# Performance work log

Hardware: AMD Instinct MI355X
Metric: run time of the kernel (lower is better)

## Reference

```python
import jax, jax.numpy as jnp
import numpy as np

N_NODES = 100000
N_EDGES = 1600000
NFEAT, NHID, NCLASS = 128, 64, 40


def setup_inputs() -> dict:
    key = jax.random.key(0)
    k = jax.random.split(key, 6)
    x = jax.random.normal(k[0], (N_NODES, NFEAT), dtype=jnp.float32)
    edge_index = jax.random.randint(k[1], (2, N_EDGES), 0, N_NODES, dtype=jnp.int64)
    edge_weight = jax.random.uniform(k[2], (N_EDGES,), dtype=jnp.float32)
    # Glorot-style init as in PyG GCNConv.reset_parameters
    W1 = jax.random.normal(k[3], (NFEAT, NHID), dtype=jnp.float32) * (1.0 / np.sqrt(NFEAT))
    b1 = jnp.zeros((NHID,), dtype=jnp.float32)
    W2 = jax.random.normal(k[4], (NHID, NCLASS), dtype=jnp.float32) * (1.0 / np.sqrt(NHID))
    b2 = jnp.zeros((NCLASS,), dtype=jnp.float32)
    return {"x": x, "edge_index": edge_index, "edge_weight": edge_weight,
            "W1": W1, "b1": b1, "W2": W2, "b2": b2}


def _gcn_conv(x, edge_index, edge_weight, W, b):
    """PyG GCNConv: add self-loops, symmetric gcn_norm, linear, scatter-add, bias."""
    n = x.shape[0]
    loop = jnp.arange(n)
    row = jnp.concatenate([edge_index[0], loop])  # source nodes
    col = jnp.concatenate([edge_index[1], loop])  # target nodes
    w = jnp.concatenate([edge_weight, jnp.ones((n,), edge_weight.dtype)])
    deg = jax.ops.segment_sum(w, col, num_segments=n)          # [N]
    dinv = jnp.where(deg > 0, jax.lax.rsqrt(deg), 0.0)
    norm = dinv[row] * w * dinv[col]                           # [E+N]
    h = x @ W                                                  # [N, out]
    msg = norm[:, None] * h[row]                               # gather: [E+N, out]
    out = jax.ops.segment_sum(msg, col, num_segments=n)        # scatter-add: [N, out]
    return out + b


def reference(x, edge_index, edge_weight, W1, b1, W2, b2):
    h = jax.nn.relu(_gcn_conv(x, edge_index, edge_weight, W1, b1))
    # F.dropout with training=False is identity (eval mode)
    return _gcn_conv(h, edge_index, edge_weight, W2, b2)
```

## Files before the change

### kernel.cpp

```cpp
#include <hip/hip_runtime.h>
#include <hip/hip_bf16.h>

#define N_NODES 100000
#define N_EDGES 1600000
#define NFEAT 128
#define NHID 64
#define NCLASS 40
#define CAP 64

#define BIN_SHIFT 9
#define BIN_NODES 512
#define NBIN ((N_NODES + BIN_NODES - 1) / BIN_NODES)
#define SCAP 10240
#define CHUNK 4096
#define EPT 16

using frag_ab = __attribute__((ext_vector_type(8))) short;
using frag_cd = __attribute__((ext_vector_type(4))) float;


__device__ __forceinline__ unsigned pack2(float a, float b) {
    unsigned ua = __float_as_uint(a), ub = __float_as_uint(b);
    unsigned ra = (ua + 0x7FFFu + ((ua >> 16) & 1u)) >> 16;
    unsigned rb = (ub + 0x7FFFu + ((ub >> 16) & 1u)) >> 16;
    return ra | (rb << 16);
}
__device__ __forceinline__ unsigned short bf16rtn(float f) {
    unsigned u = __float_as_uint(f);
    return (unsigned short)((u + 0x7FFFu + ((u >> 16) & 1u)) >> 16);
}
__device__ __forceinline__ float lo16(unsigned w) { return __uint_as_float(w << 16); }
__device__ __forceinline__ float hi16(unsigned w) { return __uint_as_float(w & 0xFFFF0000u); }


__global__ __launch_bounds__(256) void bin_kernel(const int* __restrict__ ei,
                                                  const float* __restrict__ ew,
                                                  int* __restrict__ bincnt,
                                                  uint2* __restrict__ staging) {
    __shared__ int lcnt[NBIN];
    __shared__ int gbase[NBIN];
    int t = threadIdx.x;
    for (int i = t; i < NBIN; i += 256) lcnt[i] = 0;
    __syncthreads();

    int base = blockIdx.x * CHUNK;
    int c[EPT]; unsigned en[EPT];
#pragma unroll
    for (int u = 0; u < EPT; ++u) {
        int e = base + u * 256 + t;
        if (e < N_EDGES) {
            c[u] = ei[N_EDGES + e];
            unsigned wq = (unsigned)fminf(ew[e] * 32768.0f, 32767.0f);
            en[u] = ((unsigned)ei[e] << 15) | wq;
        } else {
            c[u] = -1;
        }
    }
#pragma unroll
    for (int u = 0; u < EPT; ++u)
        if (c[u] >= 0) atomicAdd(&lcnt[c[u] >> BIN_SHIFT], 1);
    __syncthreads();
    if (t < NBIN) {
        int n = lcnt[t];
        gbase[t] = (n > 0) ? atomicAdd(&bincnt[t], n) : 0;
    }
    __syncthreads();
    if (t < NBIN) lcnt[t] = 0;
    __syncthreads();
#pragma unroll
    for (int u = 0; u < EPT; ++u) {
        if (c[u] >= 0) {
            int b = c[u] >> BIN_SHIFT;
            int p = gbase[b] + atomicAdd(&lcnt[b], 1);
            if (p < SCAP)
                staging[(size_t)b * SCAP + p] = make_uint2(en[u], (unsigned)c[u]);
        }
    }
}


__global__ __launch_bounds__(512) void place_kernel(const int* __restrict__ bincnt,
                                                    const uint2* __restrict__ staging,
                                                    unsigned* __restrict__ bucket,
                                                    int* __restrict__ cnt,
                                                    float* __restrict__ dinv) {
    __shared__ int lpos[BIN_NODES];
    __shared__ float lws[BIN_NODES];
    int b = blockIdx.x;
    int t = threadIdx.x;
    for (int i = t; i < BIN_NODES; i += 512) { lpos[i] = 0; lws[i] = 0.0f; }
    __syncthreads();

    int nodebase = b << BIN_SHIFT;
    int n = bincnt[b];
    if (n > SCAP) n = SCAP;
    const uint2* st = staging + (size_t)b * SCAP;
    for (int i = t; i < n; i += 512) {
        uint2 en = st[i];
        int local = (int)en.y - nodebase;
        int p = atomicAdd(&lpos[local], 1);
        if (p < CAP) bucket[((size_t)en.y << 6) + p] = en.x;
        atomicAdd(&lws[local], (float)(en.x & 32767u) * (1.0f / 32768.0f));
    }
    __syncthreads();
    for (int i = t; i < BIN_NODES; i += 512) {
        int node = nodebase + i;
        if (node < N_NODES) {
            cnt[node] = min(lpos[i], CAP);
            dinv[node] = rsqrtf(1.0f + lws[i]);
        }
    }
}


__global__ __launch_bounds__(256) void gemm1_kernel(const float* __restrict__ x,
                                                    const float* __restrict__ W1,
                                                    unsigned short* __restrict__ h1b) {
    __shared__ unsigned short sm[16384];
    int t = threadIdx.x;
    int row0 = blockIdx.x * 64;

#pragma unroll
    for (int p = 0; p < 4; ++p) {
        int id = p * 256 + t;
        int r = id >> 4;
        int c = id & 15;
        int gr = row0 + r; if (gr > N_NODES - 1) gr = N_NODES - 1;
        const float* src = x + (size_t)gr * NFEAT + c * 8;
        float4 f0 = *(const float4*)src;
        float4 f1 = *(const float4*)(src + 4);
        uint4 pk = make_uint4(pack2(f0.x, f0.y), pack2(f0.z, f0.w),
                              pack2(f1.x, f1.y), pack2(f1.z, f1.w));
        int cs = c ^ (r & 15);
        *(uint4*)(&sm[r * 128 + cs * 8]) = pk;
    }
#pragma unroll
    for (int p = 0; p < 4; ++p) {
        int id = p * 256 + t;
        int n = id >> 4;
        int c = id & 15;
        const float* wsrc = W1 + (size_t)(c * 8) * NHID + n;
        uint4 pk = make_uint4(pack2(wsrc[0 * NHID], wsrc[1 * NHID]),
                              pack2(wsrc[2 * NHID], wsrc[3 * NHID]),
                              pack2(wsrc[4 * NHID], wsrc[5 * NHID]),
                              pack2(wsrc[6 * NHID], wsrc[7 * NHID]));
        int cs = c ^ (n & 15);
        *(uint4*)(&sm[8192 + n * 128 + cs * 8]) = pk;
    }
    __syncthreads();

    int w = t >> 6, l = t & 63;
    int li = l & 15, q = l >> 4;
    int arow = w * 16 + li;

    frag_cd acc0 = {0.f, 0.f, 0.f, 0.f};
    frag_cd acc1 = {0.f, 0.f, 0.f, 0.f};
    frag_cd acc2 = {0.f, 0.f, 0.f, 0.f};
    frag_cd acc3 = {0.f, 0.f, 0.f, 0.f};

#pragma unroll
    for (int kc = 0; kc < 4; ++kc) {
        int cc = (kc * 4 + q) ^ li;
        frag_ab a  = *(const frag_ab*)(&sm[arow * 128 + cc * 8]);
        frag_ab b0 = *(const frag_ab*)(&sm[8192 + (0 * 16 + li) * 128 + cc * 8]);
        frag_ab b1 = *(const frag_ab*)(&sm[8192 + (1 * 16 + li) * 128 + cc * 8]);
        frag_ab b2 = *(const frag_ab*)(&sm[8192 + (2 * 16 + li) * 128 + cc * 8]);
        frag_ab b3 = *(const frag_ab*)(&sm[8192 + (3 * 16 + li) * 128 + cc * 8]);
        acc0 = __builtin_amdgcn_mfma_f32_16x16x32_bf16(a, b0, acc0, 0, 0, 0);
        acc1 = __builtin_amdgcn_mfma_f32_16x16x32_bf16(a, b1, acc1, 0, 0, 0);
        acc2 = __builtin_amdgcn_mfma_f32_16x16x32_bf16(a, b2, acc2, 0, 0, 0);
        acc3 = __builtin_amdgcn_mfma_f32_16x16x32_bf16(a, b3, acc3, 0, 0, 0);
    }

#pragma unroll
    for (int reg = 0; reg < 4; ++reg) {
        int rrow = row0 + w * 16 + q * 4 + reg;
        if (rrow < N_NODES) {
            unsigned short* dst = h1b + (size_t)rrow * NHID + li;
            dst[0]  = bf16rtn(acc0[reg]);
            dst[16] = bf16rtn(acc1[reg]);
            dst[32] = bf16rtn(acc2[reg]);
            dst[48] = bf16rtn(acc3[reg]);
        }
    }
}


__global__ __launch_bounds__(256, 4) void gather1_kernel(
        const int* __restrict__ cnt, const unsigned* __restrict__ bucket,
        const float* __restrict__ dinv, const unsigned short* __restrict__ h1b,
        const float* __restrict__ b1, unsigned short* __restrict__ relu1b) {
    int t = threadIdx.x;
    int lane = t & 63;
    int wave = t >> 6;
    int g = lane >> 3;
    int l = lane & 7;
    int node = (blockIdx.x * 4 + wave) * 8 + g;
    bool nvalid = node < N_NODES;
    int nd = nvalid ? node : N_NODES - 1;
    int d = cnt[nd];
    float dc = dinv[nd];

    uint4 eb0 = make_uint4(0u, 0u, 0u, 0u), eb1 = make_uint4(0u, 0u, 0u, 0u);
    if (l * 8 < d)     eb0 = *(const uint4*)(bucket + ((size_t)nd << 6) + l * 8);
    if (l * 8 + 4 < d) eb1 = *(const uint4*)(bucket + ((size_t)nd << 6) + l * 8 + 4);
    int rl[8]; float wl[8];
#pragma unroll
    for (int k = 0; k < 8; ++k) {
        unsigned e = (k < 4) ? ((const unsigned*)&eb0)[k] : ((const unsigned*)&eb1)[k - 4];
        int slot = l * 8 + k;
        bool ok = slot < d;
        int r = ok ? (int)(e >> 15) : 0;
        rl[k] = r;
        wl[k] = ok ? (float)(e & 32767u) * (1.0f / 32768.0f) * dinv[r] : 0.0f;
    }

    uint4 hs = *(const uint4*)(h1b + (size_t)nd * NHID + l * 8);
    float acc[8];
#pragma unroll
    for (int k = 0; k < 4; ++k) {
        unsigned w = ((const unsigned*)&hs)[k];
        acc[2 * k] = dc * lo16(w);
        acc[2 * k + 1] = dc * hi16(w);
    }

    for (int j = 0; j < d; j += 8) {
        int src = (g << 3) + (j >> 3);
        int r[8]; float w[8];
#pragma unroll
        for (int k = 0; k < 8; ++k) { r[k] = __shfl(rl[k], src); w[k] = __shfl(wl[k], src); }
        uint4 v[8];
#pragma unroll
        for (int k = 0; k < 8; ++k)
            v[k] = *(const uint4*)(h1b + (size_t)r[k] * NHID + l * 8);
#pragma unroll
        for (int k = 0; k < 8; ++k) {
#pragma unroll
            for (int q = 0; q < 4; ++q) {
                unsigned ww = ((const unsigned*)&v[k])[q];
                acc[2 * q] += w[k] * lo16(ww);
                acc[2 * q + 1] += w[k] * hi16(ww);
            }
        }
    }
    if (nvalid) {
        float4 bv0 = *(const float4*)(b1 + l * 8);
        float4 bv1 = *(const float4*)(b1 + l * 8 + 4);
        float o0 = fmaxf(dc * acc[0] + bv0.x, 0.0f), o1 = fmaxf(dc * acc[1] + bv0.y, 0.0f);
        float o2 = fmaxf(dc * acc[2] + bv0.z, 0.0f), o3 = fmaxf(dc * acc[3] + bv0.w, 0.0f);
        float o4 = fmaxf(dc * acc[4] + bv1.x, 0.0f), o5 = fmaxf(dc * acc[5] + bv1.y, 0.0f);
        float o6 = fmaxf(dc * acc[6] + bv1.z, 0.0f), o7 = fmaxf(dc * acc[7] + bv1.w, 0.0f);
        uint4 pk = make_uint4(pack2(o0, o1), pack2(o2, o3), pack2(o4, o5), pack2(o6, o7));
        *(uint4*)(relu1b + (size_t)node * NHID + l * 8) = pk;
    }
}


__global__ __launch_bounds__(256) void gemm2_kernel(const unsigned short* __restrict__ relu1b,
                                                    const float* __restrict__ W2,
                                                    unsigned short* __restrict__ h2b) {
    __shared__ unsigned short sa[64 * 64];
    __shared__ unsigned short sb[48 * 64];
    int t = threadIdx.x;
    int row0 = blockIdx.x * 64;

#pragma unroll
    for (int p = 0; p < 2; ++p) {
        int id = p * 256 + t;
        int r = id >> 3, cj = id & 7;
        int gr = row0 + r; if (gr > N_NODES - 1) gr = N_NODES - 1;
        uint4 v = *(const uint4*)(relu1b + (size_t)gr * NHID + cj * 8);
        int cs = cj ^ (r & 7);
        *(uint4*)(&sa[r * 64 + cs * 8]) = v;
    }
    for (int id = t; id < 384; id += 256) {
        int n = id >> 3, cj = id & 7;
        uint4 v = make_uint4(0u, 0u, 0u, 0u);
        if (n < NCLASS) {
            const float* wsrc = W2 + (size_t)(cj * 8) * NCLASS + n;
            v = make_uint4(pack2(wsrc[0 * NCLASS], wsrc[1 * NCLASS]),
                           pack2(wsrc[2 * NCLASS], wsrc[3 * NCLASS]),
                           pack2(wsrc[4 * NCLASS], wsrc[5 * NCLASS]),
                           pack2(wsrc[6 * NCLASS], wsrc[7 * NCLASS]));
        }
        int cs = cj ^ (n & 7);
        *(uint4*)(&sb[n * 64 + cs * 8]) = v;
    }
    __syncthreads();

    int w = t >> 6, l = t & 63;
    int li = l & 15, q = l >> 4;
    int arow = w * 16 + li;

    frag_cd acc0 = {0.f, 0.f, 0.f, 0.f};
    frag_cd acc1 = {0.f, 0.f, 0.f, 0.f};
    frag_cd acc2 = {0.f, 0.f, 0.f, 0.f};

#pragma unroll
    for (int kc = 0; kc < 2; ++kc) {
        int cc = (kc * 4 + q) ^ (li & 7);
        frag_ab a  = *(const frag_ab*)(&sa[arow * 64 + cc * 8]);
        frag_ab b0 = *(const frag_ab*)(&sb[(0 + li) * 64 + cc * 8]);
        frag_ab b1 = *(const frag_ab*)(&sb[(16 + li) * 64 + cc * 8]);
        frag_ab b2 = *(const frag_ab*)(&sb[(32 + li) * 64 + cc * 8]);
        acc0 = __builtin_amdgcn_mfma_f32_16x16x32_bf16(a, b0, acc0, 0, 0, 0);
        acc1 = __builtin_amdgcn_mfma_f32_16x16x32_bf16(a, b1, acc1, 0, 0, 0);
        acc2 = __builtin_amdgcn_mfma_f32_16x16x32_bf16(a, b2, acc2, 0, 0, 0);
    }

#pragma unroll
    for (int reg = 0; reg < 4; ++reg) {
        int rrow = row0 + w * 16 + q * 4 + reg;
        if (rrow < N_NODES) {
            unsigned short* dst = h2b + (size_t)rrow * NCLASS;
            dst[li] = bf16rtn(acc0[reg]);
            dst[16 + li] = bf16rtn(acc1[reg]);
            if (li < 8) dst[32 + li] = bf16rtn(acc2[reg]);
        }
    }
}


__global__ __launch_bounds__(256) void gather2_kernel(
        const int* __restrict__ cnt, const unsigned* __restrict__ bucket,
        const float* __restrict__ dinv, const unsigned short* __restrict__ h2b,
        const float* __restrict__ b2, float* __restrict__ out) {
    int t = threadIdx.x;
    int lane = t & 63;
    int wave = t >> 6;
    int g = lane >> 4;
    int l = lane & 15;
    int node = (blockIdx.x * 4 + wave) * 4 + g;
    bool nvalid = node < N_NODES;
    int nd = nvalid ? node : N_NODES - 1;
    int d = cnt[nd];
    float dc = dinv[nd];
    bool fvalid = (l < 10);

    uint4 eb = make_uint4(0u, 0u, 0u, 0u);
    if (l * 4 < d) eb = *(const uint4*)(bucket + ((size_t)nd << 6) + l * 4);
    int rl[4]; float wl[4];
#pragma unroll
    for (int k = 0; k < 4; ++k) {
        unsigned e = ((const unsigned*)&eb)[k];
        int slot = l * 4 + k;
        bool ok = slot < d;
        int r = ok ? (int)(e >> 15) : 0;
        rl[k] = r;
        wl[k] = ok ? (float)(e & 32767u) * (1.0f / 32768.0f) * dinv[r] : 0.0f;
    }

    float acc[4] = {};
    int lc = fvalid ? l * 4 : 0;
    if (fvalid) {
        uint2 hs = *(const uint2*)(h2b + (size_t)nd * NCLASS + lc);
        acc[0] = dc * lo16(hs.x); acc[1] = dc * hi16(hs.x);
        acc[2] = dc * lo16(hs.y); acc[3] = dc * hi16(hs.y);
    }

    for (int j = 0; j < d; j += 4) {
        int src = (g << 4) + (j >> 2);
        int r0 = __shfl(rl[0], src), r1 = __shfl(rl[1], src);
        int r2 = __shfl(rl[2], src), r3 = __shfl(rl[3], src);
        float w0 = __shfl(wl[0], src), w1 = __shfl(wl[1], src);
        float w2 = __shfl(wl[2], src), w3 = __shfl(wl[3], src);
        if (fvalid) {
            uint2 v0 = *(const uint2*)(h2b + (size_t)r0 * NCLASS + lc);
            uint2 v1 = *(const uint2*)(h2b + (size_t)r1 * NCLASS + lc);
            uint2 v2 = *(const uint2*)(h2b + (size_t)r2 * NCLASS + lc);
            uint2 v3 = *(const uint2*)(h2b + (size_t)r3 * NCLASS + lc);
            acc[0] += w0 * lo16(v0.x) + w1 * lo16(v1.x) + w2 * lo16(v2.x) + w3 * lo16(v3.x);
            acc[1] += w0 * hi16(v0.x) + w1 * hi16(v1.x) + w2 * hi16(v2.x) + w3 * hi16(v3.x);
            acc[2] += w0 * lo16(v0.y) + w1 * lo16(v1.y) + w2 * lo16(v2.y) + w3 * lo16(v3.y);
            acc[3] += w0 * hi16(v0.y) + w1 * hi16(v1.y) + w2 * hi16(v2.y) + w3 * hi16(v3.y);
        }
    }
    if (nvalid && fvalid) {
        float4 bv = *(const float4*)(b2 + l * 4);
        *(float4*)(out + (size_t)node * NCLASS + l * 4) =
            make_float4(dc * acc[0] + bv.x, dc * acc[1] + bv.y,
                        dc * acc[2] + bv.z, dc * acc[3] + bv.w);
    }
}


extern "C" void kernel_launch(void* const* d_in, const int* in_sizes, int n_in,
                              void* d_out, int out_size, void* d_ws, size_t ws_size,
                              hipStream_t stream) {
    const float* x  = (const float*)d_in[0];
    const int*   ei = (const int*)d_in[1];
    const float* ew = (const float*)d_in[2];
    const float* W1 = (const float*)d_in[3];
    const float* b1 = (const float*)d_in[4];
    const float* W2 = (const float*)d_in[5];
    const float* b2 = (const float*)d_in[6];
    float* out = (float*)d_out;

    int*            bincnt  = (int*)d_ws;
    int*            cnt     = bincnt + 256;
    float*          dinv    = (float*)(cnt + 100352);
    unsigned*       bucket  = (unsigned*)(dinv + 100352);
    unsigned short* h1b     = (unsigned short*)(bucket + (size_t)N_NODES * CAP);
    unsigned short* region2 = h1b + (size_t)N_NODES * NHID;
    uint2*          staging = (uint2*)region2;
    unsigned short* relu1b  = region2;
    unsigned short* h2b     = h1b;

    hipMemsetAsync(bincnt, 0, 256 * sizeof(int), stream);

    bin_kernel<<<(N_EDGES + CHUNK - 1) / CHUNK, 256, 0, stream>>>(ei, ew, bincnt, staging);
    place_kernel<<<NBIN, 512, 0, stream>>>(bincnt, staging, bucket, cnt, dinv);

    gemm1_kernel<<<(N_NODES + 63) / 64, 256, 0, stream>>>(x, W1, h1b);
    gather1_kernel<<<(N_NODES + 31) / 32, 256, 0, stream>>>(cnt, bucket, dinv, h1b, b1, relu1b);

    gemm2_kernel<<<(N_NODES + 63) / 64, 256, 0, stream>>>(relu1b, W2, h2b);
    gather2_kernel<<<(N_NODES + 15) / 16, 256, 0, stream>>>(cnt, bucket, dinv, h2b, b2, out);
}
```

Before: 263.1 us.

## Fuse layer-1 gather with layer-2 GEMM through shared memory

Merges the layer-1 gather/bias/ReLU kernel and the layer-2 MFMA GEMM into one kernel: each block aggregates 32 nodes, writes the bf16 ReLU rows into swizzled LDS, then runs the 64x40 GEMM on them directly. This removes the relu1b round trip through global memory and one kernel launch. In exchange every block repacks W2 into LDS, needs a block barrier after the irregular gather, and drops the 4-blocks occupancy hint while using more LDS per block. h2b now lives in the former staging/relu region instead of aliasing h1b, which the fused kernel still reads.

```diff
diff --git a/kernel.cpp b/kernel.cpp
--- a/kernel.cpp
+++ b/kernel.cpp
@@ -186,94 +186,26 @@
 }
 
 
-__global__ __launch_bounds__(256, 4) void gather1_kernel(
+__global__ __launch_bounds__(256) void g1g2_kernel(
         const int* __restrict__ cnt, const unsigned* __restrict__ bucket,
         const float* __restrict__ dinv, const unsigned short* __restrict__ h1b,
-        const float* __restrict__ b1, unsigned short* __restrict__ relu1b) {
+        const float* __restrict__ b1, const float* __restrict__ W2,
+        unsigned short* __restrict__ h2b) {
+    __shared__ unsigned short sa[32 * 64];
+    __shared__ unsigned short sb[64 * 64];
     int t = threadIdx.x;
     int lane = t & 63;
     int wave = t >> 6;
     int g = lane >> 3;
     int l = lane & 7;
-    int node = (blockIdx.x * 4 + wave) * 8 + g;
+    int row0 = blockIdx.x * 32;
+    int node = row0 + wave * 8 + g;
     bool nvalid = node < N_NODES;
     int nd = nvalid ? node : N_NODES - 1;
     int d = cnt[nd];
     float dc = dinv[nd];
 
-    uint4 eb0 = make_uint4(0u, 0u, 0u, 0u), eb1 = make_uint4(0u, 0u, 0u, 0u);
-    if (l * 8 < d)     eb0 = *(const uint4*)(bucket + ((size_t)nd << 6) + l * 8);
-    if (l * 8 + 4 < d) eb1 = *(const uint4*)(bucket + ((size_t)nd << 6) + l * 8 + 4);
-    int rl[8]; float wl[8];
-#pragma unroll
-    for (int k = 0; k < 8; ++k) {
-        unsigned e = (k < 4) ? ((const unsigned*)&eb0)[k] : ((const unsigned*)&eb1)[k - 4];
-        int slot = l * 8 + k;
-        bool ok = slot < d;
-        int r = ok ? (int)(e >> 15) : 0;
-        rl[k] = r;
-        wl[k] = ok ? (float)(e & 32767u) * (1.0f / 32768.0f) * dinv[r] : 0.0f;
-    }
-
-    uint4 hs = *(const uint4*)(h1b + (size_t)nd * NHID + l * 8);
-    float acc[8];
-#pragma unroll
-    for (int k = 0; k < 4; ++k) {
-        unsigned w = ((const unsigned*)&hs)[k];
-        acc[2 * k] = dc * lo16(w);
-        acc[2 * k + 1] = dc * hi16(w);
-    }
-
-    for (int j = 0; j < d; j += 8) {
-        int src = (g << 3) + (j >> 3);
-        int r[8]; float w[8];
-#pragma unroll
-        for (int k = 0; k < 8; ++k) { r[k] = __shfl(rl[k], src); w[k] = __shfl(wl[k], src); }
-        uint4 v[8];
-#pragma unroll
-        for (int k = 0; k < 8; ++k)
-            v[k] = *(const uint4*)(h1b + (size_t)r[k] * NHID + l * 8);
-#pragma unroll
-        for (int k = 0; k < 8; ++k) {
-#pragma unroll
-            for (int q = 0; q < 4; ++q) {
-                unsigned ww = ((const unsigned*)&v[k])[q];
-                acc[2 * q] += w[k] * lo16(ww);
-                acc[2 * q + 1] += w[k] * hi16(ww);
-            }
-        }
-    }
-    if (nvalid) {
-        float4 bv0 = *(const float4*)(b1 + l * 8);
-        float4 bv1 = *(const float4*)(b1 + l * 8 + 4);
-        float o0 = fmaxf(dc * acc[0] + bv0.x, 0.0f), o1 = fmaxf(dc * acc[1] + bv0.y, 0.0f);
-        float o2 = fmaxf(dc * acc[2] + bv0.z, 0.0f), o3 = fmaxf(dc * acc[3] + bv0.w, 0.0f);
-        float o4 = fmaxf(dc * acc[4] + bv1.x, 0.0f), o5 = fmaxf(dc * acc[5] + bv1.y, 0.0f);
-        float o6 = fmaxf(dc * acc[6] + bv1.z, 0.0f), o7 = fmaxf(dc * acc[7] + bv1.w, 0.0f);
-        uint4 pk = make_uint4(pack2(o0, o1), pack2(o2, o3), pack2(o4, o5), pack2(o6, o7));
-        *(uint4*)(relu1b + (size_t)node * NHID + l * 8) = pk;
-    }
-}
-
-
-__global__ __launch_bounds__(256) void gemm2_kernel(const unsigned short* __restrict__ relu1b,
-                                                    const float* __restrict__ W2,
-                                                    unsigned short* __restrict__ h2b) {
-    __shared__ unsigned short sa[64 * 64];
-    __shared__ unsigned short sb[48 * 64];
-    int t = threadIdx.x;
-    int row0 = blockIdx.x * 64;
-
-#pragma unroll
-    for (int p = 0; p < 2; ++p) {
-        int id = p * 256 + t;
-        int r = id >> 3, cj = id & 7;
-        int gr = row0 + r; if (gr > N_NODES - 1) gr = N_NODES - 1;
-        uint4 v = *(const uint4*)(relu1b + (size_t)gr * NHID + cj * 8);
-        int cs = cj ^ (r & 7);
-        *(uint4*)(&sa[r * 64 + cs * 8]) = v;
-    }
-    for (int id = t; id < 384; id += 256) {
+    for (int id = t; id < 512; id += 256) {
         int n = id >> 3, cj = id & 7;
         uint4 v = make_uint4(0u, 0u, 0u, 0u);
         if (n < NCLASS) {
@@ -286,36 +218,90 @@
         int cs = cj ^ (n & 7);
         *(uint4*)(&sb[n * 64 + cs * 8]) = v;
     }
-    __syncthreads();
-
-    int w = t >> 6, l = t & 63;
-    int li = l & 15, q = l >> 4;
-    int arow = w * 16 + li;
-
-    frag_cd acc0 = {0.f, 0.f, 0.f, 0.f};
-    frag_cd acc1 = {0.f, 0.f, 0.f, 0.f};
-    frag_cd acc2 = {0.f, 0.f, 0.f, 0.f};
-
+
+    uint4 eb0 = make_uint4(0u, 0u, 0u, 0u), eb1 = make_uint4(0u, 0u, 0u, 0u);
+    if (l * 8 < d)     eb0 = *(const uint4*)(bucket + ((size_t)nd << 6) + l * 8);
+    if (l * 8 + 4 < d) eb1 = *(const uint4*)(bucket + ((size_t)nd << 6) + l * 8 + 4);
+    int rl[8]; float wl[8];
+#pragma unroll
+    for (int k = 0; k < 8; ++k) {
+        unsigned e = (k < 4) ? ((const unsigned*)&eb0)[k] : ((const unsigned*)&eb1)[k - 4];
+        int sl = l * 8 + k;
+        bool ok = sl < d;
+        int r = ok ? (int)(e >> 15) : 0;
+        rl[k] = r;
+        wl[k] = ok ? (float)(e & 32767u) * (1.0f / 32768.0f) * dinv[r] : 0.0f;
+    }
+
+    uint4 hs = *(const uint4*)(h1b + (size_t)nd * NHID + l * 8);
+    float acc[8];
+#pragma unroll
+    for (int k = 0; k < 4; ++k) {
+        unsigned w = ((const unsigned*)&hs)[k];
+        acc[2 * k] = dc * lo16(w);
+        acc[2 * k + 1] = dc * hi16(w);
+    }
+
+    for (int j = 0; j < d; j += 8) {
+        int src = (g << 3) + (j >> 3);
+        int r[8]; float w[8];
+#pragma unroll
+        for (int k = 0; k < 8; ++k) { r[k] = __shfl(rl[k], src); w[k] = __shfl(wl[k], src); }
+        uint4 v[8];
+#pragma unroll
+        for (int k = 0; k < 8; ++k)
+            v[k] = *(const uint4*)(h1b + (size_t)r[k] * NHID + l * 8);
+#pragma unroll
+        for (int k = 0; k < 8; ++k) {
+#pragma unroll
+            for (int q = 0; q < 4; ++q) {
+                unsigned ww = ((const unsigned*)&v[k])[q];
+                acc[2 * q] += w[k] * lo16(ww);
+                acc[2 * q + 1] += w[k] * hi16(ww);
+            }
+        }
+    }
+
+    {
+        float4 bv0 = *(const float4*)(b1 + l * 8);
+        float4 bv1 = *(const float4*)(b1 + l * 8 + 4);
+        float o0 = fmaxf(dc * acc[0] + bv0.x, 0.0f), o1 = fmaxf(dc * acc[1] + bv0.y, 0.0f);
+        float o2 = fmaxf(dc * acc[2] + bv0.z, 0.0f), o3 = fmaxf(dc * acc[3] + bv0.w, 0.0f);
+        float o4 = fmaxf(dc * acc[4] + bv1.x, 0.0f), o5 = fmaxf(dc * acc[5] + bv1.y, 0.0f);
+        float o6 = fmaxf(dc * acc[6] + bv1.z, 0.0f), o7 = fmaxf(dc * acc[7] + bv1.w, 0.0f);
+        uint4 pk = make_uint4(pack2(o0, o1), pack2(o2, o3), pack2(o4, o5), pack2(o6, o7));
+        int r = wave * 8 + g;
+        int cs = l ^ (r & 7);
+        *(uint4*)(&sa[r * 64 + cs * 8]) = pk;
+    }
+    __syncthreads();
+
+    int li = lane & 15, q = lane >> 4;
+    int arow = (wave & 1) * 16 + li;
+    int ct0 = (wave >> 1) * 2;
+
+    frag_cd c0 = {0.f, 0.f, 0.f, 0.f};
+    frag_cd c1 = {0.f, 0.f, 0.f, 0.f};
 #pragma unroll
     for (int kc = 0; kc < 2; ++kc) {
         int cc = (kc * 4 + q) ^ (li & 7);
-        frag_ab a  = *(const frag_ab*)(&sa[arow * 64 + cc * 8]);
-        frag_ab b0 = *(const frag_ab*)(&sb[(0 + li) * 64 + cc * 8]);
-        frag_ab b1 = *(const frag_ab*)(&sb[(16 + li) * 64 + cc * 8]);
-        frag_ab b2 = *(const frag_ab*)(&sb[(32 + li) * 64 + cc * 8]);
-        acc0 = __builtin_amdgcn_mfma_f32_16x16x32_bf16(a, b0, acc0, 0, 0, 0);
-        acc1 = __builtin_amdgcn_mfma_f32_16x16x32_bf16(a, b1, acc1, 0, 0, 0);
-        acc2 = __builtin_amdgcn_mfma_f32_16x16x32_bf16(a, b2, acc2, 0, 0, 0);
+        frag_ab a   = *(const frag_ab*)(&sa[arow * 64 + cc * 8]);
+        frag_ab b0f = *(const frag_ab*)(&sb[(ct0 * 16 + li) * 64 + cc * 8]);
+        frag_ab b1f = *(const frag_ab*)(&sb[((ct0 + 1) * 16 + li) * 64 + cc * 8]);
+        c0 = __builtin_amdgcn_mfma_f32_16x16x32_bf16(a, b0f, c0, 0, 0, 0);
+        c1 = __builtin_amdgcn_mfma_f32_16x16x32_bf16(a, b1f, c1, 0, 0, 0);
     }
 
 #pragma unroll
     for (int reg = 0; reg < 4; ++reg) {
-        int rrow = row0 + w * 16 + q * 4 + reg;
-        if (rrow < N_NODES) {
-            unsigned short* dst = h2b + (size_t)rrow * NCLASS;
-            dst[li] = bf16rtn(acc0[reg]);
-            dst[16 + li] = bf16rtn(acc1[reg]);
-            if (li < 8) dst[32 + li] = bf16rtn(acc2[reg]);
+        int rr = (wave & 1) * 16 + q * 4 + reg;
+        int onode = row0 + rr;
+        if (onode < N_NODES) {
+            unsigned short* dst = h2b + (size_t)onode * NCLASS;
+            int col0 = ct0 * 16 + li;
+            int col1 = (ct0 + 1) * 16 + li;
+            if (col0 < NCLASS) dst[col0] = bf16rtn(c0[reg]);
+            if (col1 < NCLASS) dst[col1] = bf16rtn(c1[reg]);
         }
     }
 }
@@ -403,8 +389,7 @@
     unsigned short* h1b     = (unsigned short*)(bucket + (size_t)N_NODES * CAP);
     unsigned short* region2 = h1b + (size_t)N_NODES * NHID;
     uint2*          staging = (uint2*)region2;
-    unsigned short* relu1b  = region2;
-    unsigned short* h2b     = h1b;
+    unsigned short* h2b     = region2;
 
     hipMemsetAsync(bincnt, 0, 256 * sizeof(int), stream);
 
@@ -412,8 +397,9 @@
     place_kernel<<<NBIN, 512, 0, stream>>>(bincnt, staging, bucket, cnt, dinv);
 
     gemm1_kernel<<<(N_NODES + 63) / 64, 256, 0, stream>>>(x, W1, h1b);
-    gather1_kernel<<<(N_NODES + 31) / 32, 256, 0, stream>>>(cnt, bucket, dinv, h1b, b1, relu1b);
-
-    gemm2_kernel<<<(N_NODES + 63) / 64, 256, 0, stream>>>(relu1b, W2, h2b);
+
+    g1g2_kernel<<<(N_NODES + 31) / 32, 256, 0, stream>>>(
+        cnt, bucket, dinv, h1b, b1, W2, h2b);
+
     gather2_kernel<<<(N_NODES + 15) / 16, 256, 0, stream>>>(cnt, bucket, dinv, h2b, b2, out);
 }
```

After: 256.3 us. 2.6% less time.
